# Optimization experiments

Measured on AMD Instinct MI355X. Metric: run time of the kernel, lower is better.

Reference implementation:

```python
import jax, jax.numpy as jnp
import numpy as np
from jax import lax

T, B, H_IN, H_HID = 2048, 64, 256, 256


def _orth(key, shape):
    a = jax.random.normal(key, shape, jnp.float32)
    if shape[0] >= shape[1]:
        q, _ = jnp.linalg.qr(a)
    else:
        q, _ = jnp.linalg.qr(a.T)
        q = q.T
    return q[: shape[0], : shape[1]].astype(jnp.float32)


def setup_inputs() -> dict:
    key = jax.random.key(0)
    ks = jax.random.split(key, 6)
    x = jax.random.normal(ks[0], (T, B, H_IN), jnp.float32)
    rnn_hxs = jax.random.normal(ks[1], (1, B, H_HID), jnp.float32)
    batch_mask = jax.random.randint(ks[2], (T, B), 0, 2).astype(bool)
    # force column 0 fully valid so pad_packed max length == T (static shape)
    batch_mask = batch_mask.at[:, 0].set(True)
    w_ih = _orth(ks[3], (3 * H_HID, H_IN))   # [3H, H_in] gates r,z,n
    w_hh = _orth(ks[4], (3 * H_HID, H_HID))
    b_ih = jnp.zeros((3 * H_HID,), jnp.float32)  # constant_(0) init
    b_hh = jnp.zeros((3 * H_HID,), jnp.float32)
    return {"x": x, "rnn_hxs": rnn_hxs, "batch_mask": batch_mask,
            "w_ih": w_ih, "w_hh": w_hh, "b_ih": b_ih, "b_hh": b_hh}


def _gru_ragged(x, h0, batch_mask, w_ih, w_hh, b_ih, b_hh):
    Tn, Bn, _ = x.shape
    Hh = h0.shape[-1]
    mask = batch_mask
    lens = mask.sum(0)                      # [B] per-column valid lengths
    # --- gather/pack: move valid steps of each column to the front ---
    rank = jnp.cumsum(mask, axis=0) - mask  # compact position per (t,b)
    rank_m = jnp.where(mask, rank, Tn)      # invalid rows -> dump row Tn
    cols = jnp.broadcast_to(jnp.arange(Bn), (Tn, Bn))
    compact = jnp.zeros((Tn + 1, Bn, x.shape[-1]), x.dtype)
    compact = compact.at[rank_m, cols].set(x)[:Tn]
    # --- GRU over compact sequences; h frozen past each column's length ---
    gi = jnp.einsum('tbi,gi->tbg', compact, w_ih) + b_ih  # [T,B,3H]
    valid = jnp.arange(Tn)[:, None] < lens[None, :]       # [T,B]

    def step(h, inp):
        gi_t, v = inp
        gh = jnp.einsum('bh,gh->bg', h, w_hh) + b_hh
        r = jax.nn.sigmoid(gi_t[:, :Hh] + gh[:, :Hh])
        z = jax.nn.sigmoid(gi_t[:, Hh:2 * Hh] + gh[:, Hh:2 * Hh])
        n = jnp.tanh(gi_t[:, 2 * Hh:] + r * gh[:, 2 * Hh:])
        h_new = (1.0 - z) * n + z * h
        h_out = jnp.where(v[:, None], h_new, h)
        out = jnp.where(v[:, None], h_new, 0.0)  # pad_packed zero padding
        return h_out, out

    hT, scores = lax.scan(step, h0, (gi, valid))  # scores [T,B,Hh]
    # --- masked_scatter: true positions of dest (row-major t,b order)
    # consume consecutive H-rows of the flattened padded scores ---
    mflat = mask.reshape(-1)
    flat_rank = jnp.cumsum(mflat) - mflat            # exclusive cumsum
    src = scores.reshape(Tn * Bn, Hh)
    gathered = src[flat_rank]                        # [T*B, Hh]
    out = jnp.where(mflat[:, None], gathered, 0.0).reshape(Tn, Bn, Hh)
    return out, hT


def reference(x, rnn_hxs, batch_mask, w_ih, w_hh, b_ih, b_hh):
    scores, hT = _gru_ragged(x, rnn_hxs[0], batch_mask, w_ih, w_hh, b_ih, b_hh)
    return scores, hT[None]
```

## Files before the change

### kernel.cpp

```cpp
#include <hip/hip_runtime.h>
#include <cstdint>
#include <cstddef>

#define T_LEN 2048
#define B_N   64
#define H_INP 256
#define H_HID 256
#define G3    768
#define M_ROWS (T_LEN * B_N)
#define SCH   8

typedef _Float16 f16;
typedef _Float16 f16x2 __attribute__((ext_vector_type(2)));
typedef _Float16 f16x8 __attribute__((ext_vector_type(8)));
typedef float    f32x4 __attribute__((ext_vector_type(4)));

static __device__ __forceinline__ void gldl16(const void* g, void* ldsbase, void* ldsexact) {
#if __has_builtin(__builtin_amdgcn_global_load_lds)
  __builtin_amdgcn_global_load_lds((const __attribute__((address_space(1))) void*)g,
                                   (__attribute__((address_space(3))) void*)ldsbase, 16, 0, 0);
  (void)ldsexact;
#else
  *(uint4*)ldsexact = *(const uint4*)g;
#endif
}

__global__ void k_zero(float4* __restrict__ p, int n4) {
  int i = blockIdx.x * blockDim.x + threadIdx.x;
  int stride = gridDim.x * blockDim.x;
  float4 z; z.x = z.y = z.z = z.w = 0.f;
  for (; i < n4; i += stride) p[i] = z;
}

__global__ void k_cvt(const float2* __restrict__ s, f16x2* __restrict__ d, int n2) {
  int i = blockIdx.x * blockDim.x + threadIdx.x;
  int stride = gridDim.x * blockDim.x;
  for (; i < n2; i += stride) {
    float2 v = s[i];
    f16x2 p; p.x = (f16)v.x; p.y = (f16)v.y;
    d[i] = p;
  }
}

__global__ __launch_bounds__(64) void k_prep_col(const int* __restrict__ mask,
                                                 unsigned short* __restrict__ tidx,
                                                 int* __restrict__ lens) {
  const int b = blockIdx.x;
  const int lane = threadIdx.x;
  unsigned short* tp = tidx + b * T_LEN;
  int base = 0;
  for (int c = 0; c < T_LEN / 64; ++c) {
    int t = c * 64 + lane;
    bool m = mask[t * B_N + b] != 0;
    unsigned long long bal = __ballot(m);
    int pc = __popcll(bal & ((1ull << lane) - 1ull));
    if (m) tp[base + pc] = (unsigned short)t;
    base += __popcll(bal);
  }
  if (lane == 0) lens[b] = base;
}

__global__ __launch_bounds__(256) void k_rowcnt(const int* __restrict__ mask,
                                                int* __restrict__ rowcnt) {
  int g = blockIdx.x * 256 + threadIdx.x;
  int t = g >> 6, lane = g & 63;
  bool m = mask[t * B_N + lane] != 0;
  unsigned long long bal = __ballot(m);
  if (lane == 0) rowcnt[t] = __popcll(bal);
}

__global__ __launch_bounds__(512) void k_rowpref(const int* __restrict__ rowcnt,
                                                 int* __restrict__ rowpref,
                                                 int* __restrict__ ntru) {
  const int tid = threadIdx.x;
  const int lane = tid & 63, w = tid >> 6;
  int4 v = ((const int4*)rowcnt)[tid];
  int s = v.x + v.y + v.z + v.w;
  int incl = s;
  for (int d = 1; d < 64; d <<= 1) {
    int t = __shfl_up(incl, d, 64);
    if (lane >= d) incl += t;
  }
  __shared__ int wt[8], wo[8];
  if (lane == 63) wt[w] = incl;
  __syncthreads();
  if (tid == 0) {
    int run = 0;
    for (int i = 0; i < 8; ++i) { wo[i] = run; run += wt[i]; }
    ntru[0] = run;
  }
  __syncthreads();
  int base = wo[w] + incl - s;
  int4 o; o.x = base; o.y = base + v.x; o.z = o.y + v.y; o.w = o.z + v.z;
  ((int4*)rowpref)[tid] = o;
}

__global__ __launch_bounds__(256) void k_inv(const int* __restrict__ mask,
                                             const int* __restrict__ rowpref,
                                             int* __restrict__ inv) {
  int g = blockIdx.x * 256 + threadIdx.x;
  int t = g >> 6, lane = g & 63;
  bool m = mask[t * B_N + lane] != 0;
  unsigned long long bal = __ballot(m);
  int r = rowpref[t] + __popcll(bal & ((1ull << lane) - 1ull));
  if (m) inv[r] = t * B_N + lane;
}

__global__ __launch_bounds__(256) void k_invT(const int* __restrict__ inv,
                                              const int* __restrict__ ntru,
                                              int* __restrict__ invT) {
  int j = blockIdx.x * 256 + threadIdx.x;
  int v = (j < ntru[0]) ? inv[j] : -1;
  invT[(j & 63) * T_LEN + (j >> 6)] = v;
}

__global__ __launch_bounds__(256) void k_gemm(const f16* __restrict__ X,
                                              const f16* __restrict__ W,
                                              const float* __restrict__ bias,
                                              f16* __restrict__ GI) {
  const int lane = threadIdx.x & 63;
  const int wave = threadIdx.x >> 6;
  const int m0 = blockIdx.x * 64 + wave * 16;
  const int n0 = blockIdx.y * 64;
  const int idx16 = lane & 15;
  const int kofs  = (lane >> 4) * 8;

  __shared__ __align__(16) f16 st[4][16][72];

  const f16* ap  = X + (size_t)(m0 + idx16) * H_INP + kofs;
  const f16* bp0 = W + (size_t)(n0 + idx16) * H_INP + kofs;

  f32x4 acc[4] = { {0,0,0,0}, {0,0,0,0}, {0,0,0,0}, {0,0,0,0} };
#pragma unroll
  for (int kt = 0; kt < 8; ++kt) {
    f16x8 a = *(const f16x8*)(ap + kt * 32);
#pragma unroll
    for (int nt = 0; nt < 4; ++nt) {
      f16x8 bb = *(const f16x8*)(bp0 + (size_t)nt * 16 * H_INP + kt * 32);
      acc[nt] = __builtin_amdgcn_mfma_f32_16x16x32_f16(a, bb, acc[nt], 0, 0, 0);
    }
  }
#pragma unroll
  for (int nt = 0; nt < 4; ++nt) {
    const int col = nt * 16 + idx16;
    const float bv = bias[n0 + col];
#pragma unroll
    for (int r = 0; r < 4; ++r)
      st[wave][(lane >> 4) * 4 + r][col] = (f16)(acc[nt][r] + bv);
  }
  {
    const int row = lane >> 2, seg = lane & 3;
    const uint4* sp = (const uint4*)&st[wave][row][seg * 16];
    uint4 v0 = sp[0], v1 = sp[1];
    uint4* gp = (uint4*)(GI + (size_t)(m0 + row) * G3 + n0 + seg * 16);
    gp[0] = v0; gp[1] = v1;
  }
}

__global__ __launch_bounds__(256)
__attribute__((amdgpu_waves_per_eu(1, 1)))
void k_scan(const f16* __restrict__ Whh,
            const f16* __restrict__ GI,
            const float* __restrict__ h0,
            const float* __restrict__ bhh,
            const unsigned short* __restrict__ tidx,
            const int* __restrict__ lens,
            const int* __restrict__ invT,
            float* __restrict__ out) {
  const int b = blockIdx.x;
  const int tid = threadIdx.x;
  const int w = tid >> 6;
  const int lane = tid & 63;
  const int g = lane >> 4;
  const int c = lane & 15;

  __shared__ __align__(16) f16   GIbuf[2][SCH * G3];
  __shared__ __align__(16) float outb[2][SCH * H_HID];
  __shared__ __align__(16) float ghs[G3];
  __shared__ __align__(16) f16   hf[2][H_HID];
  __shared__ unsigned short tcol[T_LEN];
  __shared__ int      invcol[T_LEN];

  const int L = lens[b];

  f16x8 wA[96];
#pragma unroll
  for (int i = 0; i < 12; ++i) {
    const f16* wp = Whh + (size_t)((w + 4 * i) * 16 + c) * H_HID + g * 8;
#pragma unroll
    for (int kt = 0; kt < 8; ++kt)
      wA[i * 8 + kt] = *(const f16x8*)(wp + kt * 32);
  }

  const int j = (w + 4 * g) * 16 + c;
  const float bh0 = bhh[j];
  const float bh1 = bhh[H_HID + j];
  const float bh2 = bhh[2 * H_HID + j];

  for (int i = tid; i < T_LEN; i += 256) {
    tcol[i] = tidx[b * T_LEN + i];
    invcol[i] = invT[b * T_LEN + i];
  }
  float h_reg = h0[b * H_HID + j];
  hf[0][j] = (f16)h_reg;
  __syncthreads();

  const char* GIc = (const char*)GI;
  const int wavbase = w << 10;

  auto issue_chunk = [&](int m) {
#pragma unroll
    for (int rnd = 0; rnd < 3; ++rnd) {
      int p = rnd * 4096 + tid * 16;
      int r = p / 1536;
      int kk = m * SCH + r;
      int t = tcol[kk < L ? kk : 0] & (T_LEN - 1);
      const char* src = GIc + ((size_t)((t << 6) + b)) * 1536 + (p - r * 1536);
      char* dbase = (char*)GIbuf[m & 1] + rnd * 4096 + wavbase;
      gldl16(src, dbase, (char*)GIbuf[m & 1] + p);
    }
  };

  issue_chunk(0);
  __syncthreads();

  const f32x4 z4 = {0.f, 0.f, 0.f, 0.f};

  const int nchunks = (L + SCH - 1) >> 3;
  for (int n = 0; n < nchunks; ++n) {
    const int par = n & 1;
    if (n + 1 < nchunks) issue_chunk(n + 1);
    if (n > 0) {
      int r = tid >> 5, c8 = (tid & 31) << 3;
      int kk = (n - 1) * SCH + r;
      if (kk < L) {
        int iv = invcol[kk];
        if (iv >= 0) {
          const float* sb = &outb[par ^ 1][r * H_HID + c8];
          float* gp = out + (size_t)iv * H_HID + c8;
          *(float4*)gp = *(const float4*)sb;
          *(float4*)(gp + 4) = *(const float4*)(sb + 4);
        }
      }
    }

    const int kbase = n * SCH;
    const int smax = (L - kbase < SCH) ? (L - kbase) : SCH;
    for (int s = 0; s < smax; ++s) {
      const int rd = (kbase + s) & 1;
      f16x8 bf[8];
#pragma unroll
      for (int kt = 0; kt < 8; ++kt)
        bf[kt] = *(const f16x8*)(&hf[rd][kt * 32 + g * 8]);
#pragma unroll
      for (int half = 0; half < 2; ++half) {
        f32x4 acc[6];
#pragma unroll
        for (int i = 0; i < 6; ++i)
          acc[i] = __builtin_amdgcn_mfma_f32_16x16x32_f16(
              wA[(half * 6 + i) * 8], bf[0], z4, 0, 0, 0);
#pragma unroll
        for (int kt = 1; kt < 8; ++kt)
#pragma unroll
          for (int i = 0; i < 6; ++i)
            acc[i] = __builtin_amdgcn_mfma_f32_16x16x32_f16(
                wA[(half * 6 + i) * 8 + kt], bf[kt], acc[i], 0, 0, 0);
        if (c == 0) {
#pragma unroll
          for (int i = 0; i < 6; ++i)
            *(f32x4*)(&ghs[(w + 4 * (half * 6 + i)) * 16 + g * 4]) = acc[i];
        }
      }
      {
        const f16* gib = GIbuf[par] + s * G3;
        const float gi0 = (float)gib[j];
        const float gi1 = (float)gib[H_HID + j];
        const float gi2 = (float)gib[2 * H_HID + j];
        const float ghr = ghs[j] + bh0;
        const float ghz = ghs[H_HID + j] + bh1;
        const float ghn = ghs[2 * H_HID + j] + bh2;
        const float rg = __builtin_amdgcn_rcpf(1.f + __expf(-(gi0 + ghr)));
        const float zg = __builtin_amdgcn_rcpf(1.f + __expf(-(gi1 + ghz)));
        const float xx = gi2 + rg * ghn;
        const float ng = 1.f - 2.f * __builtin_amdgcn_rcpf(1.f + __expf(2.f * xx));
        const float hn = (1.f - zg) * ng + zg * h_reg;
        h_reg = hn;
        hf[rd ^ 1][j] = (f16)hn;
        outb[par][s * H_HID + j] = hn;
      }
      __syncthreads();
    }
  }
  if (L > 0) {
    const int nc = nchunks - 1;
    int r = tid >> 5, c8 = (tid & 31) << 3;
    int kk = nc * SCH + r;
    if (kk < L) {
      int iv = invcol[kk];
      if (iv >= 0) {
        const float* sb = &outb[nc & 1][r * H_HID + c8];
        float* gp = out + (size_t)iv * H_HID + c8;
        *(float4*)gp = *(const float4*)sb;
        *(float4*)(gp + 4) = *(const float4*)(sb + 4);
      }
    }
  }
  out[(size_t)M_ROWS * H_HID + (size_t)b * H_HID + j] = h_reg;
}

extern "C" void kernel_launch(void* const* d_in, const int* in_sizes, int n_in,
                              void* d_out, int out_size, void* d_ws, size_t ws_size,
                              hipStream_t stream) {
  const float* x    = (const float*)d_in[0];
  const float* h0   = (const float*)d_in[1];
  const int*   mask = (const int*)d_in[2];
  const float* wih  = (const float*)d_in[3];
  const float* whh  = (const float*)d_in[4];
  const float* bih  = (const float*)d_in[5];
  const float* bhh  = (const float*)d_in[6];
  float* out = (float*)d_out;

  char* ws = (char*)d_ws;
  f16* X16   = (f16*)(ws + 0);
  int* invT  = (int*)(ws + 0);
  f16* Wih16 = (f16*)(ws + 67108864);
  f16* Whh16 = (f16*)(ws + 67502080);
  f16* GI    = (f16*)(ws + 67895296);
  unsigned short* tidx = (unsigned short*)(ws + 269221888);
  int* rowcnt  = (int*)(ws + 269484032);
  int* rowpref = (int*)(ws + 269492224);
  int* inv   = (int*)(ws + 269746176);
  int* lens  = (int*)(ws + 270270464);
  int* ntru  = (int*)(ws + 270270720);

  hipLaunchKernelGGL(k_zero, dim3(4096), dim3(256), 0, stream,
                     (float4*)d_out, out_size / 4);
  hipLaunchKernelGGL(k_cvt, dim3(4096), dim3(256), 0, stream,
                     (const float2*)x, (f16x2*)X16, M_ROWS * H_INP / 2);
  hipLaunchKernelGGL(k_cvt, dim3(96), dim3(256), 0, stream,
                     (const float2*)wih, (f16x2*)Wih16, G3 * H_INP / 2);
  hipLaunchKernelGGL(k_cvt, dim3(96), dim3(256), 0, stream,
                     (const float2*)whh, (f16x2*)Whh16, G3 * H_INP / 2);
  hipLaunchKernelGGL(k_prep_col, dim3(B_N), dim3(64), 0, stream,
                     mask, tidx, lens);
  hipLaunchKernelGGL(k_rowcnt, dim3(512), dim3(256), 0, stream, mask, rowcnt);
  hipLaunchKernelGGL(k_rowpref, dim3(1), dim3(512), 0, stream,
                     rowcnt, rowpref, ntru);
  hipLaunchKernelGGL(k_inv, dim3(512), dim3(256), 0, stream,
                     mask, rowpref, inv);
  hipLaunchKernelGGL(k_gemm, dim3(M_ROWS / 64, G3 / 64), dim3(256), 0, stream,
                     X16, Wih16, bih, GI);
  hipLaunchKernelGGL(k_invT, dim3(512), dim3(256), 0, stream,
                     inv, ntru, invT);
  hipLaunchKernelGGL(k_scan, dim3(B_N), dim3(256), 0, stream,
                     Whh16, GI, h0, bhh, tidx, lens, invT, out);
}
```

Measured before the change: 3.801 ms.

## Split GRU scan recurrence across 8 waves per block with halved weight registers

```diff
diff --git a/kernel.cpp b/kernel.cpp
--- a/kernel.cpp
+++ b/kernel.cpp
@@ -157,8 +157,8 @@
   }
 }
 
-__global__ __launch_bounds__(256)
-__attribute__((amdgpu_waves_per_eu(1, 1)))
+__global__ __launch_bounds__(512)
+__attribute__((amdgpu_waves_per_eu(2, 2)))
 void k_scan(const f16* __restrict__ Whh,
             const f16* __restrict__ GI,
             const float* __restrict__ h0,
@@ -173,6 +173,7 @@
   const int lane = tid & 63;
   const int g = lane >> 4;
   const int c = lane & 15;
+  const int hi = g & 1;
 
   __shared__ __align__(16) f16   GIbuf[2][SCH * G3];
   __shared__ __align__(16) float outb[2][SCH * H_HID];
@@ -183,40 +184,49 @@
 
   const int L = lens[b];
 
-  f16x8 wA[96];
-#pragma unroll
-  for (int i = 0; i < 12; ++i) {
-    const f16* wp = Whh + (size_t)((w + 4 * i) * 16 + c) * H_HID + g * 8;
+  f16x8 wA[48];
+#pragma unroll
+  for (int i = 0; i < 6; ++i) {
+    const f16* wp = Whh + (size_t)((w + 8 * i) * 16 + c) * H_HID + g * 8;
 #pragma unroll
     for (int kt = 0; kt < 8; ++kt)
       wA[i * 8 + kt] = *(const f16x8*)(wp + kt * 32);
   }
 
-  const int j = (w + 4 * g) * 16 + c;
+  const int j = (w + 8 * hi) * 16 + c;
   const float bh0 = bhh[j];
   const float bh1 = bhh[H_HID + j];
   const float bh2 = bhh[2 * H_HID + j];
 
-  for (int i = tid; i < T_LEN; i += 256) {
+  for (int i = tid; i < T_LEN; i += 512) {
     tcol[i] = tidx[b * T_LEN + i];
     invcol[i] = invT[b * T_LEN + i];
   }
-  float h_reg = h0[b * H_HID + j];
-  hf[0][j] = (f16)h_reg;
+  float h_reg = 0.f;
+  if (lane < 32) h_reg = h0[b * H_HID + j];
+  if (tid < H_HID) hf[0][tid] = (f16)h0[b * H_HID + tid];
   __syncthreads();
 
   const char* GIc = (const char*)GI;
   const int wavbase = w << 10;
 
   auto issue_chunk = [&](int m) {
-#pragma unroll
-    for (int rnd = 0; rnd < 3; ++rnd) {
-      int p = rnd * 4096 + tid * 16;
+    {
+      int p = tid << 4;
       int r = p / 1536;
       int kk = m * SCH + r;
       int t = tcol[kk < L ? kk : 0] & (T_LEN - 1);
       const char* src = GIc + ((size_t)((t << 6) + b)) * 1536 + (p - r * 1536);
-      char* dbase = (char*)GIbuf[m & 1] + rnd * 4096 + wavbase;
+      char* dbase = (char*)GIbuf[m & 1] + wavbase;
+      gldl16(src, dbase, (char*)GIbuf[m & 1] + p);
+    }
+    if (tid < 256) {
+      int p = 8192 + (tid << 4);
+      int r = p / 1536;
+      int kk = m * SCH + r;
+      int t = tcol[kk < L ? kk : 0] & (T_LEN - 1);
+      const char* src = GIc + ((size_t)((t << 6) + b)) * 1536 + (p - r * 1536);
+      char* dbase = (char*)GIbuf[m & 1] + 8192 + wavbase;
       gldl16(src, dbase, (char*)GIbuf[m & 1] + p);
     }
   };
@@ -231,16 +241,13 @@
     const int par = n & 1;
     if (n + 1 < nchunks) issue_chunk(n + 1);
     if (n > 0) {
-      int r = tid >> 5, c8 = (tid & 31) << 3;
+      int r = tid >> 6, c4 = (tid & 63) << 2;
       int kk = (n - 1) * SCH + r;
       if (kk < L) {
         int iv = invcol[kk];
-        if (iv >= 0) {
-          const float* sb = &outb[par ^ 1][r * H_HID + c8];
-          float* gp = out + (size_t)iv * H_HID + c8;
-          *(float4*)gp = *(const float4*)sb;
-          *(float4*)(gp + 4) = *(const float4*)(sb + 4);
-        }
+        if (iv >= 0)
+          *(float4*)(out + (size_t)iv * H_HID + c4) =
+              *(const float4*)(outb[par ^ 1] + r * H_HID + c4);
       }
     }
 
@@ -248,30 +255,27 @@
     const int smax = (L - kbase < SCH) ? (L - kbase) : SCH;
     for (int s = 0; s < smax; ++s) {
       const int rd = (kbase + s) & 1;
-      f16x8 bf[8];
-#pragma unroll
-      for (int kt = 0; kt < 8; ++kt)
-        bf[kt] = *(const f16x8*)(&hf[rd][kt * 32 + g * 8]);
-#pragma unroll
-      for (int half = 0; half < 2; ++half) {
-        f32x4 acc[6];
+      const f16* hb = hf[rd] + g * 8;
+      f16x8 b_cur = *(const f16x8*)(hb);
+      f16x8 b_nxt = *(const f16x8*)(hb + 32);
+      f32x4 acc[6];
+#pragma unroll
+      for (int i = 0; i < 6; ++i)
+        acc[i] = __builtin_amdgcn_mfma_f32_16x16x32_f16(wA[i * 8], b_cur, z4, 0, 0, 0);
+#pragma unroll
+      for (int kt = 1; kt < 8; ++kt) {
+        b_cur = b_nxt;
+        if (kt < 7) b_nxt = *(const f16x8*)(hb + (kt + 1) * 32);
 #pragma unroll
         for (int i = 0; i < 6; ++i)
-          acc[i] = __builtin_amdgcn_mfma_f32_16x16x32_f16(
-              wA[(half * 6 + i) * 8], bf[0], z4, 0, 0, 0);
-#pragma unroll
-        for (int kt = 1; kt < 8; ++kt)
-#pragma unroll
-          for (int i = 0; i < 6; ++i)
-            acc[i] = __builtin_amdgcn_mfma_f32_16x16x32_f16(
-                wA[(half * 6 + i) * 8 + kt], bf[kt], acc[i], 0, 0, 0);
-        if (c == 0) {
-#pragma unroll
-          for (int i = 0; i < 6; ++i)
-            *(f32x4*)(&ghs[(w + 4 * (half * 6 + i)) * 16 + g * 4]) = acc[i];
-        }
+          acc[i] = __builtin_amdgcn_mfma_f32_16x16x32_f16(wA[i * 8 + kt], b_cur, acc[i], 0, 0, 0);
       }
-      {
+      if (c == 0) {
+#pragma unroll
+        for (int i = 0; i < 6; ++i)
+          *(f32x4*)(&ghs[(w + 8 * i) * 16 + g * 4]) = acc[i];
+      }
+      if (lane < 32) {
         const f16* gib = GIbuf[par] + s * G3;
         const float gi0 = (float)gib[j];
         const float gi1 = (float)gib[H_HID + j];
@@ -293,19 +297,17 @@
   }
   if (L > 0) {
     const int nc = nchunks - 1;
-    int r = tid >> 5, c8 = (tid & 31) << 3;
+    int r = tid >> 6, c4 = (tid & 63) << 2;
     int kk = nc * SCH + r;
     if (kk < L) {
       int iv = invcol[kk];
-      if (iv >= 0) {
-        const float* sb = &outb[nc & 1][r * H_HID + c8];
-        float* gp = out + (size_t)iv * H_HID + c8;
-        *(float4*)gp = *(const float4*)sb;
-        *(float4*)(gp + 4) = *(const float4*)(sb + 4);
-      }
-    }
-  }
-  out[(size_t)M_ROWS * H_HID + (size_t)b * H_HID + j] = h_reg;
+      if (iv >= 0)
+        *(float4*)(out + (size_t)iv * H_HID + c4) =
+            *(const float4*)(outb[nc & 1] + r * H_HID + c4);
+    }
+  }
+  if (lane < 32)
+    out[(size_t)M_ROWS * H_HID + (size_t)b * H_HID + j] = h_reg;
 }
 
 extern "C" void kernel_launch(void* const* d_in, const int* in_sizes, int n_in,
@@ -352,6 +354,6 @@
                      X16, Wih16, bih, GI);
   hipLaunchKernelGGL(k_invT, dim3(512), dim3(256), 0, stream,
                      inv, ntru, invT);
-  hipLaunchKernelGGL(k_scan, dim3(B_N), dim3(256), 0, stream,
+  hipLaunchKernelGGL(k_scan, dim3(B_N), dim3(512), 0, stream,
                      Whh16, GI, h0, bhh, tidx, lens, invT, out);
 }
```

Result: faster. 3.304 ms (-13.1%).
